# Kernel tuning notes

Measured on AMD Instinct MI355X. Metric: run time of the kernel, lower is better.

## Reference

```python
import jax, jax.numpy as jnp
import numpy as np

RF = 512      # receptive field (power of 2)
F = 128       # filter_size
UP = 200      # upsample_size
MGC = 60      # mgc_size
NB = 4        # num_blocks
NL = 9        # log2(RF) CondConv layers per WaveNet block
T = 4         # number of mgc frames
N = T * UP    # number of sliding windows (800)
SQ = 0.70710678118


def setup_inputs() -> dict:
    key = jax.random.key(0)
    ks = jax.random.split(key, 12)
    r = lambda k, shp, s: jax.random.normal(k, shp, jnp.float32) * s
    return {
        "mgc": r(ks[0], (T, MGC), 1.0),
        "signal": r(ks[1], (N + RF,), 0.5),
        "cond_w": r(ks[2], (MGC * UP, MGC), 0.1),
        "cond_b": jnp.zeros((MGC * UP,), jnp.float32),
        "conv0_w": r(ks[3], (NB, 3, F, 1, 2), 0.3),
        "conv0_b": jnp.zeros((NB, 3, F), jnp.float32),
        "convL_w": r(ks[4], (NB, NL - 1, 3, F, F, 2), 0.08),
        "convL_b": jnp.zeros((NB, NL - 1, 3, F), jnp.float32),
        "condlin_w": r(ks[5], (NB, NL, 2, F, MGC), 0.1),
        "condlin_b": jnp.zeros((NB, NL, 2, F), jnp.float32),
        "pre_w": r(ks[6], (NB, 256, F), 0.08),
        "pre_b": jnp.zeros((NB, 256), jnp.float32),
        "mean_w": r(ks[7], (NB, 1, 256), 0.05),
        "mean_b": jnp.zeros((NB, 1), jnp.float32),
        "std_w": r(ks[8], (NB, 1, 256), 0.05),
        "std_b": jnp.zeros((NB, 1), jnp.float32),
        "eps": r(ks[9], (NB, N, 1), 1.0),
    }


def _cond_conv(h, W, b, cw, cb, cond):
    # h: [N, Cin, L]; W: [3, F, Cin, 2] (input/gate/residual stacked); b: [3, F]
    # kernel=2, stride=2 -> non-overlapping pairs; express as einsum GEMM
    n, c, L = h.shape
    hr = h.reshape(n, c, L // 2, 2)
    o = jnp.einsum('nclk,tock->tnol', hr, W) + b[:, None, :, None]  # [3, N, F, L/2]
    ci = cond @ cw[0].T + cb[0]  # [N, F]
    cg = cond @ cw[1].T + cb[1]  # [N, F]
    it = jnp.tanh(o[0] + ci[:, :, None])
    gt = jax.nn.sigmoid(o[1] + cg[:, :, None])
    return (it * gt + o[2]) * SQ


def _forward(mgc, signal, cond_w, cond_b, conv0_w, conv0_b, convL_w, convL_b,
             condlin_w, condlin_b, pre_w, pre_b, mean_w, mean_b, std_w, std_b, eps):
    # conditioning: Linear(60 -> 60*200) + tanh, reshaped to [T*200, 60]
    cond = jnp.tanh(mgc @ cond_w.T + cond_b).reshape(N, MGC)
    idx = jnp.arange(N)[:, None] + jnp.arange(RF)[None, :]  # sliding windows
    prev = signal
    tails = []
    mean = logvar = None
    for blk in range(NB):
        h = prev[idx][:, None, :]  # [N, 1, RF]
        for l in range(NL):
            W = conv0_w[blk] if l == 0 else convL_w[blk, l - 1]
            bb = conv0_b[blk] if l == 0 else convL_b[blk, l - 1]
            h = _cond_conv(h, W, bb, condlin_w[blk, l], condlin_b[blk, l], cond)
        pre = jax.nn.relu(h[:, :, 0] @ pre_w[blk].T + pre_b[blk])  # [N, 256]
        mean = pre @ mean_w[blk].T + mean_b[blk]    # [N, 1]
        logvar = pre @ std_w[blk].T + std_b[blk]    # [N, 1]
        new_x = eps[blk] * jnp.exp(0.5 * logvar) + mean  # reparameterize
        tails.append(jax.lax.stop_gradient(new_x[-RF:]))  # detached tail
        prev = jnp.concatenate([signal[:RF], new_x[:, 0]])
    return signal[RF:], mean, logvar, jnp.stack(tails)


def reference(mgc, signal, cond_w, cond_b, conv0_w, conv0_b, convL_w, convL_b,
              condlin_w, condlin_b, pre_w, pre_b, mean_w, mean_b, std_w, std_b, eps):
    return _forward(mgc, signal, cond_w, cond_b, conv0_w, conv0_b, convL_w, convL_b,
                    condlin_w, condlin_b, pre_w, pre_b, mean_w, mean_b, std_w, std_b, eps)
```

## Files before the change

kernel.cpp:

```cpp
#include <hip/hip_runtime.h>
#include <hip/hip_bf16.h>

#define F 128
#define MGCS 60
#define NWIN 800
#define RFS 512
#define NBLK 4
#define NLAY 9
#define SQF 0.70710678118f

typedef __attribute__((ext_vector_type(8))) short s16x8;
typedef __attribute__((ext_vector_type(4))) float f32x4;

#define VMCNT(n) asm volatile("s_waitcnt vmcnt(" #n ")" ::: "memory")

__device__ __forceinline__ float gated_act(float o0, float o1, float o2) {
  o0 = fminf(fmaxf(o0, -21.f), 21.f);
  o1 = fminf(fmaxf(o1, -21.f), 21.f);
  float a = __expf(2.f * o0);
  float b = __expf(-o1);
  float r = (a - 1.f) * __builtin_amdgcn_rcpf((a + 1.f) * (1.f + b));
  return (r + o2) * SQF;
}


__global__ void k_cond(const float* __restrict__ mgc, const float* __restrict__ cond_w,
                       const float* __restrict__ cond_b, float* __restrict__ cond) {
  int i = blockIdx.x * blockDim.x + threadIdx.x;
  if (i >= NWIN * MGCS) return;
  int n = i / MGCS, m = i % MGCS;
  int t = n / 200, u = n % 200;
  const float* wrow = cond_w + (size_t)(u * MGCS + m) * MGCS;
  const float* mr = mgc + t * MGCS;
  float s = cond_b[u * MGCS + m];
#pragma unroll
  for (int k = 0; k < MGCS; ++k) s += mr[k] * wrow[k];
  cond[i] = tanhf(s);
}

__global__ __launch_bounds__(256) void k_ci(
    const float* __restrict__ cond, const float* __restrict__ clw,
    const float* __restrict__ clb, float* __restrict__ CI) {
  int w = blockIdx.x;
  int n0 = blockIdx.y * 128;
  __shared__ float wsh[128][61];
  __shared__ float csh[128][61];
  int tid = threadIdx.x;
  for (int idx = tid; idx < 128 * MGCS; idx += 256) {
    int f = idx / MGCS, k = idx % MGCS;
    wsh[f][k] = clw[((size_t)w * 128 + f) * MGCS + k];
  }
  for (int idx = tid; idx < 128 * MGCS; idx += 256) {
    int n = idx / MGCS, k = idx % MGCS;
    csh[n][k] = (n0 + n < NWIN) ? cond[(n0 + n) * MGCS + k] : 0.f;
  }
  __syncthreads();
  int tn = tid >> 4, tf = tid & 15;
  float acc[8][8] = {};
  for (int k = 0; k < MGCS; ++k) {
    float a[8], b[8];
#pragma unroll
    for (int i = 0; i < 8; ++i) a[i] = csh[i * 16 + tn][k];
#pragma unroll
    for (int j = 0; j < 8; ++j) b[j] = wsh[j * 16 + tf][k];
#pragma unroll
    for (int i = 0; i < 8; ++i)
#pragma unroll
      for (int j = 0; j < 8; ++j) acc[i][j] += a[i] * b[j];
  }
  float bb[8];
#pragma unroll
  for (int j = 0; j < 8; ++j) bb[j] = clb[w * 128 + j * 16 + tf];
#pragma unroll
  for (int i = 0; i < 8; ++i) {
    int n = n0 + i * 16 + tn;
    if (n < NWIN) {
#pragma unroll
      for (int j = 0; j < 8; ++j)
        CI[((size_t)w * NWIN + n) * 128 + j * 16 + tf] = acc[i][j] + bb[j];
    }
  }
}

__global__ void k_wt(const float* __restrict__ convL_w, __hip_bfloat16* __restrict__ W2) {
  int i = blockIdx.x * blockDim.x + threadIdx.x;
  const int total = NBLK * 8 * 384 * 256;
  if (i >= total) return;
  int k = i & 255;
  int tf = (i >> 8) % 384;
  int wl = i / (384 * 256);
  int t = tf >> 7, f = tf & 127;
  int k2 = k >> 7, c = k & 127;
  W2[i] = __float2bfloat16(convL_w[(((size_t)(wl * 3 + t) * 128 + f) * 128 + c) * 2 + k2]);
}

__global__ void k_wt2(const float* __restrict__ pre_w, __hip_bfloat16* __restrict__ PW) {
  int i = blockIdx.x * blockDim.x + threadIdx.x;
  if (i < NBLK * 256 * 128) PW[i] = __float2bfloat16(pre_w[i]);
}

__global__ void k_outsig(const float* __restrict__ signal, float* __restrict__ out) {
  int i = blockIdx.x * blockDim.x + threadIdx.x;
  if (i < NWIN) out[i] = signal[RFS + i];
}


__global__ void k_pre0(const float* __restrict__ prev, const float* __restrict__ w0,
                       const float* __restrict__ b0, float* __restrict__ CV) {
  int i = blockIdx.x * blockDim.x + threadIdx.x;
  if (i >= 1310 * 384) return;
  int tf = i % 384, s = i / 384;
  CV[i] = b0[tf] + prev[s] * w0[tf * 2] + prev[s + 1] * w0[tf * 2 + 1];
}

__global__ void k_layer0(const float* __restrict__ CV, const float* __restrict__ CIb,
                         __hip_bfloat16* __restrict__ out) {
  int i = blockIdx.x * blockDim.x + threadIdx.x;
  if (i >= NWIN * 256 * 16) return;
  int fg = i & 15;
  int rest = i >> 4;
  int j = rest & 255;
  int n = rest >> 8;
  int f0 = fg * 8;
  const float* cv = CV + (size_t)(n + 2 * j) * 384;
  const float* ci = CIb + (size_t)n * F;
  float4 c0a = *(const float4*)(cv + f0),       c0b = *(const float4*)(cv + f0 + 4);
  float4 c1a = *(const float4*)(cv + 128 + f0), c1b = *(const float4*)(cv + 132 + f0);
  float4 c2a = *(const float4*)(cv + 256 + f0), c2b = *(const float4*)(cv + 260 + f0);
  float4 i0a = *(const float4*)(ci + f0),       i0b = *(const float4*)(ci + f0 + 4);
  float4 i1a = *(const float4*)(ci + (size_t)NWIN * F + f0);
  float4 i1b = *(const float4*)(ci + (size_t)NWIN * F + f0 + 4);
  s16x8 res;
#pragma unroll
  for (int e = 0; e < 8; ++e) {
    float o0 = ((e < 4) ? (&c0a.x)[e] : (&c0b.x)[e - 4]) + ((e < 4) ? (&i0a.x)[e] : (&i0b.x)[e - 4]);
    float o1 = ((e < 4) ? (&c1a.x)[e] : (&c1b.x)[e - 4]) + ((e < 4) ? (&i1a.x)[e] : (&i1b.x)[e - 4]);
    float o2 = (e < 4) ? (&c2a.x)[e] : (&c2b.x)[e - 4];
    __hip_bfloat16 h = __float2bfloat16(gated_act(o0, o1, o2));
    res[e] = *(short*)&h;
  }
  *(s16x8*)(out + ((size_t)(n * 256 + j)) * F + f0) = res;
}

template <int MFR, int FF, bool FLAT>
__device__ __forceinline__ void fuse_layer(
    const char* src, char* dst, const char* Wb, const float* __restrict__ bb,
    const float* __restrict__ ciA, const float* __restrict__ ciB,
    int n0, int logLW, int MV, int mbase, int fbase, int lane) {
  const int col = lane & 15, kg = lane >> 4;
  f32x4 acc[MFR][FF][3];
#pragma unroll
  for (int mf = 0; mf < MFR; ++mf)
#pragma unroll
    for (int ff = 0; ff < FF; ++ff)
#pragma unroll
      for (int g = 0; g < 3; ++g) acc[mf][ff][g] = (f32x4)(0.f);
#pragma unroll
  for (int ks = 0; ks < 8; ++ks) {
    s16x8 breg[FF][3];
#pragma unroll
    for (int ff = 0; ff < FF; ++ff)
#pragma unroll
      for (int g = 0; g < 3; ++g) {
        int tf = g * 128 + fbase + ff * 16 + col;
        breg[ff][g] = *(const s16x8*)(Wb + (size_t)tf * 512 + ks * 64 + kg * 16);
      }
    s16x8 afr[MFR];
#pragma unroll
    for (int mf = 0; mf < MFR; ++mf) {
      int row = mbase + mf * 16 + col;
      row = row < MV ? row : MV - 1;
      afr[mf] = *(const s16x8*)(src + row * 512 + ((ks * 64 + kg * 16) ^ ((row & 7) << 4)));
    }
#pragma unroll
    for (int ff = 0; ff < FF; ++ff)
#pragma unroll
      for (int g = 0; g < 3; ++g)
#pragma unroll
        for (int mf = 0; mf < MFR; ++mf)
          acc[mf][ff][g] = __builtin_amdgcn_mfma_f32_16x16x32_bf16(afr[mf], breg[ff][g], acc[mf][ff][g], 0, 0, 0);
  }
#pragma unroll
  for (int mf = 0; mf < MFR; ++mf)
#pragma unroll
    for (int ff = 0; ff < FF; ++ff) {
      int f = fbase + ff * 16 + col;
      float b0 = bb[f], b1 = bb[128 + f], b2 = bb[256 + f];
#pragma unroll
      for (int r = 0; r < 4; ++r) {
        int orow = mbase + mf * 16 + kg * 4 + r;
        if (orow < MV) {
          int n = n0 + (orow >> logLW);
          float o0 = acc[mf][ff][0][r] + b0 + ciA[n * 128 + f];
          float o1 = acc[mf][ff][1][r] + b1 + ciB[n * 128 + f];
          float o2 = acc[mf][ff][2][r] + b2;
          __hip_bfloat16 h = __float2bfloat16(gated_act(o0, o1, o2));
          if (FLAT) {
            *(short*)(dst + orow * 256 + ((f * 2) ^ ((orow & 7) << 4))) = *(short*)&h;
          } else {
            int trow = ((orow >> logLW) << (logLW - 1)) | ((orow & ((1 << logLW) - 1)) >> 1);
            int kb = ((orow & 1) * 128 + f) * 2;
            *(short*)(dst + trow * 512 + (kb ^ ((trow & 7) << 4))) = *(short*)&h;
          }
        }
      }
    }
}

__global__ __launch_bounds__(512, 1) void k_fuse12(
    const __hip_bfloat16* __restrict__ A0, const __hip_bfloat16* __restrict__ W2b,
    const float* __restrict__ cb, const float* __restrict__ CIb,
    __hip_bfloat16* __restrict__ outC) {
  __shared__ char Ain[128 * 512];
  __shared__ char Bp[64 * 512];
  const int n = blockIdx.x;
  const int tid = threadIdx.x;
  const int lane = tid & 63, wid = tid >> 6;
  const char* srcg = (const char*)A0 + (size_t)n * 65536;
  const int half = lane >> 5, lin = (lane & 31) * 16;
#pragma unroll
  for (int it = 0; it < 8; ++it) {
    int inst = wid * 8 + it;
    int row = inst * 2 + half;
    __builtin_amdgcn_global_load_lds(
        (const __attribute__((address_space(1))) unsigned int*)(srcg + row * 512 + (lin ^ ((row & 7) << 4))),
        (__attribute__((address_space(3))) unsigned int*)(Ain + inst * 1024), 16, 0, 0);
  }
  VMCNT(0);
  __syncthreads();
  const int fbase = wid * 16;
  const char* W0 = (const char*)W2b;
  const char* W1 = (const char*)W2b + (size_t)384 * 512;
  const float* c1A = CIb + (size_t)(1 * 2 + 0) * NWIN * F;
  const float* c1B = CIb + (size_t)(1 * 2 + 1) * NWIN * F;
  const float* c2A = CIb + (size_t)(2 * 2 + 0) * NWIN * F;
  const float* c2B = CIb + (size_t)(2 * 2 + 1) * NWIN * F;
  fuse_layer<4, 1, false>(Ain, Bp, W0, cb, c1A, c1B, n, 7, 128, 0, fbase, lane);
  fuse_layer<4, 1, false>(Ain, Bp, W0, cb, c1A, c1B, n, 7, 128, 64, fbase, lane);
  __syncthreads();
  fuse_layer<4, 1, true>(Bp, Ain, W1, cb + 384, c2A, c2B, n, 6, 64, 0, fbase, lane);
  __syncthreads();
#pragma unroll
  for (int p = 0; p < 2; ++p) {
    int idx = p * 512 + tid;
    int row = idx >> 4;
    int off = (idx & 15) * 16;
    s16x8 v = *(const s16x8*)(Ain + row * 256 + (off ^ ((row & 7) << 4)));
    *(s16x8*)((char*)outC + (size_t)n * 16384 + row * 256 + off) = v;
  }
}

__global__ __launch_bounds__(256, 1) void k_tail6(
    const __hip_bfloat16* __restrict__ C2, const __hip_bfloat16* __restrict__ W2b,
    const float* __restrict__ cb, const float* __restrict__ CIb,
    const __hip_bfloat16* __restrict__ PWb, const float* __restrict__ pb_,
    const float* __restrict__ mw_, const float* __restrict__ mb_,
    const float* __restrict__ sw_, const float* __restrict__ sb_,
    const float* __restrict__ eps_, const float* __restrict__ signal,
    float* __restrict__ prev_next, float* __restrict__ out_mean,
    float* __restrict__ out_logvar, float* __restrict__ out_tails) {
  __shared__ char Ain[128 * 512];
  __shared__ char Bp[64 * 512];
  __shared__ float psm[4][256];
  __shared__ float psv[4][256];
  const int b = blockIdx.x, n0 = b * 4;
  const int tid = threadIdx.x;
  const int lane = tid & 63, wid = tid >> 6;
  const int col = lane & 15, kg = lane >> 4;
  const char* srcg = (const char*)C2 + (size_t)n0 * 16384;
  const int half = lane >> 5, lin = (lane & 31) * 16;
#pragma unroll
  for (int it = 0; it < 16; ++it) {
    int inst = wid * 16 + it;
    int row = inst * 2 + half;
    __builtin_amdgcn_global_load_lds(
        (const __attribute__((address_space(1))) unsigned int*)(srcg + row * 512 + (lin ^ ((row & 7) << 4))),
        (__attribute__((address_space(3))) unsigned int*)(Ain + inst * 1024), 16, 0, 0);
  }
  VMCNT(0);
  __syncthreads();
  const int fbase = wid * 32;
#define WLp(lm) ((const char*)W2b + (size_t)(lm) * 384 * 512)
#define CIL(l, t) (CIb + (size_t)((l) * 2 + (t)) * NWIN * F)
  fuse_layer<4, 2, false>(Ain, Bp, WLp(2), cb + 2 * 384, CIL(3, 0), CIL(3, 1), n0, 5, 128, 0, fbase, lane);
  fuse_layer<4, 2, false>(Ain, Bp, WLp(2), cb + 2 * 384, CIL(3, 0), CIL(3, 1), n0, 5, 128, 64, fbase, lane);
  __syncthreads();
  fuse_layer<4, 2, false>(Bp, Ain, WLp(3), cb + 3 * 384, CIL(4, 0), CIL(4, 1), n0, 4, 64, 0, fbase, lane);
  __syncthreads();
  fuse_layer<2, 2, false>(Ain, Bp, WLp(4), cb + 4 * 384, CIL(5, 0), CIL(5, 1), n0, 3, 32, 0, fbase, lane);
  __syncthreads();
  fuse_layer<1, 2, false>(Bp, Ain, WLp(5), cb + 5 * 384, CIL(6, 0), CIL(6, 1), n0, 2, 16, 0, fbase, lane);
  __syncthreads();
  fuse_layer<1, 2, false>(Ain, Bp, WLp(6), cb + 6 * 384, CIL(7, 0), CIL(7, 1), n0, 1, 8, 0, fbase, lane);
  __syncthreads();
  fuse_layer<1, 2, true>(Bp, Ain, WLp(7), cb + 7 * 384, CIL(8, 0), CIL(8, 1), n0, 0, 4, 0, fbase, lane);
  __syncthreads();

  {
    f32x4 acc2[4];
#pragma unroll
    for (int nf = 0; nf < 4; ++nf) acc2[nf] = (f32x4)(0.f);
    const char* PB = (const char*)PWb;
    int row = col < 4 ? col : 3;
#pragma unroll
    for (int ks = 0; ks < 4; ++ks) {
      s16x8 afr = *(const s16x8*)(Ain + row * 256 + ((ks * 64 + kg * 16) ^ ((row & 7) << 4)));
#pragma unroll
      for (int nf = 0; nf < 4; ++nf) {
        int o = wid * 64 + nf * 16 + col;
        s16x8 bfr = *(const s16x8*)(PB + (size_t)o * 256 + ks * 64 + kg * 16);
        acc2[nf] = __builtin_amdgcn_mfma_f32_16x16x32_bf16(afr, bfr, acc2[nf], 0, 0, 0);
      }
    }
#pragma unroll
    for (int nf = 0; nf < 4; ++nf) {
      int o = wid * 64 + nf * 16 + col;
      float pb = pb_[o], mw = mw_[o], sw = sw_[o];
#pragma unroll
      for (int r = 0; r < 4; ++r) {
        int m = kg * 4 + r;
        if (m < 4) {
          float p = fmaxf(acc2[nf][r] + pb, 0.f);
          psm[m][o] = p * mw;
          psv[m][o] = p * sw;
        }
      }
    }
  }
  __syncthreads();
  {
    float sm = 0.f, sv = 0.f;
#pragma unroll
    for (int e = 0; e < 4; ++e) {
      sm += psm[wid][lane * 4 + e];
      sv += psv[wid][lane * 4 + e];
    }
#pragma unroll
    for (int off = 32; off > 0; off >>= 1) {
      sm += __shfl_down(sm, off);
      sv += __shfl_down(sv, off);
    }
    if (lane == 0) {
      int nn = n0 + wid;
      float mean = sm + mb_[0];
      float logv = sv + sb_[0];
      float nx = eps_[nn] * expf(0.5f * logv) + mean;
      if (prev_next) prev_next[RFS + nn] = nx;
      if (out_mean) { out_mean[nn] = mean; out_logvar[nn] = logv; }
      if (nn >= NWIN - RFS) out_tails[nn - (NWIN - RFS)] = nx;
    }
  }
  if (prev_next && tid < 4 && n0 + tid < RFS)
    prev_next[n0 + tid] = signal[n0 + tid];
}


extern "C" void kernel_launch(void* const* d_in, const int* in_sizes, int n_in,
                              void* d_out, int out_size, void* d_ws, size_t ws_size,
                              hipStream_t stream) {
  const float* mgc      = (const float*)d_in[0];
  const float* signal   = (const float*)d_in[1];
  const float* cond_w   = (const float*)d_in[2];
  const float* cond_b   = (const float*)d_in[3];
  const float* conv0_w  = (const float*)d_in[4];
  const float* conv0_b  = (const float*)d_in[5];
  const float* convL_w  = (const float*)d_in[6];
  const float* convL_b  = (const float*)d_in[7];
  const float* condlin_w= (const float*)d_in[8];
  const float* condlin_b= (const float*)d_in[9];
  const float* pre_w    = (const float*)d_in[10];
  const float* pre_b    = (const float*)d_in[11];
  const float* mean_w   = (const float*)d_in[12];
  const float* mean_b   = (const float*)d_in[13];
  const float* std_w    = (const float*)d_in[14];
  const float* std_b    = (const float*)d_in[15];
  const float* eps      = (const float*)d_in[16];
  float* out = (float*)d_out;

  float* wsf   = (float*)d_ws;
  float* cond  = wsf;
  float* CI    = cond + 48000;
  float* prevb = CI + 7372800;
  float* CV    = prevb + 5248;
  float* base  = CV + 503040;
  __hip_bfloat16* W2   = (__hip_bfloat16*)base;
  __hip_bfloat16* PW   = W2 + 3145728;
  __hip_bfloat16* bufA = PW + 131072;
  __hip_bfloat16* bufC = bufA + 26214400 + 65536;

  k_cond<<<(NWIN * MGCS + 255) / 256, 256, 0, stream>>>(mgc, cond_w, cond_b, cond);
  k_ci<<<dim3(72, 7), 256, 0, stream>>>(cond, condlin_w, condlin_b, CI);
  k_wt<<<(NBLK * 8 * 384 * 256 + 255) / 256, 256, 0, stream>>>(convL_w, W2);
  k_wt2<<<(NBLK * 256 * 128 + 255) / 256, 256, 0, stream>>>(pre_w, PW);
  k_outsig<<<(NWIN + 255) / 256, 256, 0, stream>>>(signal, out);

  for (int blk = 0; blk < NBLK; ++blk) {
    const float* prev = (blk == 0) ? signal : (prevb + (size_t)(blk - 1) * 1312);
    const float* CIb = CI + (size_t)(blk * NLAY) * 2 * NWIN * F;
    k_pre0<<<(1310 * 384 + 255) / 256, 256, 0, stream>>>(
        prev, conv0_w + (size_t)blk * 3 * F * 2, conv0_b + (size_t)blk * 3 * F, CV);
    k_layer0<<<(NWIN * 256 * 16 + 255) / 256, 256, 0, stream>>>(CV, CIb, bufA);

    k_fuse12<<<NWIN, 512, 0, stream>>>(
        bufA, W2 + (size_t)blk * 8 * 384 * 256, convL_b + (size_t)blk * 8 * 384, CIb, bufC);

    k_tail6<<<NWIN / 4, 256, 0, stream>>>(
        bufC, W2 + (size_t)blk * 8 * 384 * 256,
        convL_b + (size_t)blk * 8 * 384, CIb,
        PW + (size_t)blk * 256 * 128, pre_b + (size_t)blk * 256,
        mean_w + (size_t)blk * 256, mean_b + blk,
        std_w + (size_t)blk * 256, std_b + blk,
        eps + (size_t)blk * NWIN, signal,
        (blk < 3) ? (prevb + (size_t)blk * 1312) : nullptr,
        (blk == 3) ? (out + 800) : nullptr,
        (blk == 3) ? (out + 1600) : nullptr,
        out + 2400 + (size_t)blk * 512);
  }
}
```

Before: 677.9 us.

## Fuse layer0 gated activation into fused kernel and halve per-block work

Removes the standalone layer0 kernel and computes its gated activation directly into shared memory inside a new k_fuse012 kernel. This avoids writing and re-reading a large bf16 intermediate buffer in global memory. Each window is now split across two blocks with half-size LDS tiles so more blocks fit per CU. The tail kernel likewise processes two windows per block instead of four, giving more blocks and higher occupancy bounds. The cost is duplicated weight loads across the extra blocks and more launch-level parallelism overhead.

```diff
diff --git a/kernel.cpp b/kernel.cpp
--- a/kernel.cpp
+++ b/kernel.cpp
@@ -111,35 +111,6 @@
   if (i >= 1310 * 384) return;
   int tf = i % 384, s = i / 384;
   CV[i] = b0[tf] + prev[s] * w0[tf * 2] + prev[s + 1] * w0[tf * 2 + 1];
-}
-
-__global__ void k_layer0(const float* __restrict__ CV, const float* __restrict__ CIb,
-                         __hip_bfloat16* __restrict__ out) {
-  int i = blockIdx.x * blockDim.x + threadIdx.x;
-  if (i >= NWIN * 256 * 16) return;
-  int fg = i & 15;
-  int rest = i >> 4;
-  int j = rest & 255;
-  int n = rest >> 8;
-  int f0 = fg * 8;
-  const float* cv = CV + (size_t)(n + 2 * j) * 384;
-  const float* ci = CIb + (size_t)n * F;
-  float4 c0a = *(const float4*)(cv + f0),       c0b = *(const float4*)(cv + f0 + 4);
-  float4 c1a = *(const float4*)(cv + 128 + f0), c1b = *(const float4*)(cv + 132 + f0);
-  float4 c2a = *(const float4*)(cv + 256 + f0), c2b = *(const float4*)(cv + 260 + f0);
-  float4 i0a = *(const float4*)(ci + f0),       i0b = *(const float4*)(ci + f0 + 4);
-  float4 i1a = *(const float4*)(ci + (size_t)NWIN * F + f0);
-  float4 i1b = *(const float4*)(ci + (size_t)NWIN * F + f0 + 4);
-  s16x8 res;
-#pragma unroll
-  for (int e = 0; e < 8; ++e) {
-    float o0 = ((e < 4) ? (&c0a.x)[e] : (&c0b.x)[e - 4]) + ((e < 4) ? (&i0a.x)[e] : (&i0b.x)[e - 4]);
-    float o1 = ((e < 4) ? (&c1a.x)[e] : (&c1b.x)[e - 4]) + ((e < 4) ? (&i1a.x)[e] : (&i1b.x)[e - 4]);
-    float o2 = (e < 4) ? (&c2a.x)[e] : (&c2b.x)[e - 4];
-    __hip_bfloat16 h = __float2bfloat16(gated_act(o0, o1, o2));
-    res[e] = *(short*)&h;
-  }
-  *(s16x8*)(out + ((size_t)(n * 256 + j)) * F + f0) = res;
 }
 
 template <int MFR, int FF, bool FLAT>
@@ -207,50 +178,64 @@
     }
 }
 
-__global__ __launch_bounds__(512, 1) void k_fuse12(
-    const __hip_bfloat16* __restrict__ A0, const __hip_bfloat16* __restrict__ W2b,
+#define CIL(l, t) (CIb + (size_t)((l) * 2 + (t)) * NWIN * F)
+
+__global__ __launch_bounds__(512, 4) void k_fuse012(
+    const float* __restrict__ CV, const __hip_bfloat16* __restrict__ W2b,
     const float* __restrict__ cb, const float* __restrict__ CIb,
     __hip_bfloat16* __restrict__ outC) {
-  __shared__ char Ain[128 * 512];
-  __shared__ char Bp[64 * 512];
-  const int n = blockIdx.x;
+  __shared__ char Ain[64 * 512];
+  __shared__ char Bp[32 * 512];
+  const int bx = blockIdx.x;
+  const int n = bx >> 1, c = bx & 1;
   const int tid = threadIdx.x;
   const int lane = tid & 63, wid = tid >> 6;
-  const char* srcg = (const char*)A0 + (size_t)n * 65536;
-  const int half = lane >> 5, lin = (lane & 31) * 16;
-#pragma unroll
-  for (int it = 0; it < 8; ++it) {
-    int inst = wid * 8 + it;
-    int row = inst * 2 + half;
-    __builtin_amdgcn_global_load_lds(
-        (const __attribute__((address_space(1))) unsigned int*)(srcg + row * 512 + (lin ^ ((row & 7) << 4))),
-        (__attribute__((address_space(3))) unsigned int*)(Ain + inst * 1024), 16, 0, 0);
-  }
-  VMCNT(0);
-  __syncthreads();
+
+  {
+    const int jl = tid >> 2;
+    const int f0 = (tid & 3) * 32;
+    const float* cv = CV + (size_t)(n + 2 * (c * 128 + jl)) * 384;
+    const float* ci0 = CIL(0, 0) + n * 128;
+    const float* ci1 = CIL(0, 1) + n * 128;
+    const int row = jl >> 1;
+    const int kbase = (jl & 1) * 128;
+#pragma unroll
+    for (int e8 = 0; e8 < 4; ++e8) {
+      int f = f0 + e8 * 8;
+      float4 a0 = *(const float4*)(cv + f),       a1 = *(const float4*)(cv + f + 4);
+      float4 b0 = *(const float4*)(cv + 128 + f), b1 = *(const float4*)(cv + 132 + f);
+      float4 g0 = *(const float4*)(cv + 256 + f), g1 = *(const float4*)(cv + 260 + f);
+      float4 i0 = *(const float4*)(ci0 + f),      i0b = *(const float4*)(ci0 + f + 4);
+      float4 i1 = *(const float4*)(ci1 + f),      i1b = *(const float4*)(ci1 + f + 4);
+      s16x8 res;
+#pragma unroll
+      for (int e = 0; e < 8; ++e) {
+        float o0 = ((e < 4) ? (&a0.x)[e] : (&a1.x)[e - 4]) + ((e < 4) ? (&i0.x)[e] : (&i0b.x)[e - 4]);
+        float o1 = ((e < 4) ? (&b0.x)[e] : (&b1.x)[e - 4]) + ((e < 4) ? (&i1.x)[e] : (&i1b.x)[e - 4]);
+        float o2 = (e < 4) ? (&g0.x)[e] : (&g1.x)[e - 4];
+        __hip_bfloat16 h = __float2bfloat16(gated_act(o0, o1, o2));
+        res[e] = *(short*)&h;
+      }
+      *(s16x8*)(Ain + row * 512 + (((kbase + f) * 2) ^ ((row & 7) << 4))) = res;
+    }
+  }
+  __syncthreads();
+
   const int fbase = wid * 16;
-  const char* W0 = (const char*)W2b;
-  const char* W1 = (const char*)W2b + (size_t)384 * 512;
-  const float* c1A = CIb + (size_t)(1 * 2 + 0) * NWIN * F;
-  const float* c1B = CIb + (size_t)(1 * 2 + 1) * NWIN * F;
-  const float* c2A = CIb + (size_t)(2 * 2 + 0) * NWIN * F;
-  const float* c2B = CIb + (size_t)(2 * 2 + 1) * NWIN * F;
-  fuse_layer<4, 1, false>(Ain, Bp, W0, cb, c1A, c1B, n, 7, 128, 0, fbase, lane);
-  fuse_layer<4, 1, false>(Ain, Bp, W0, cb, c1A, c1B, n, 7, 128, 64, fbase, lane);
-  __syncthreads();
-  fuse_layer<4, 1, true>(Bp, Ain, W1, cb + 384, c2A, c2B, n, 6, 64, 0, fbase, lane);
-  __syncthreads();
-#pragma unroll
-  for (int p = 0; p < 2; ++p) {
-    int idx = p * 512 + tid;
-    int row = idx >> 4;
-    int off = (idx & 15) * 16;
-    s16x8 v = *(const s16x8*)(Ain + row * 256 + (off ^ ((row & 7) << 4)));
-    *(s16x8*)((char*)outC + (size_t)n * 16384 + row * 256 + off) = v;
-  }
-}
-
-__global__ __launch_bounds__(256, 1) void k_tail6(
+  fuse_layer<4, 1, false>(Ain, Bp, (const char*)W2b, cb,
+                          CIL(1, 0), CIL(1, 1), n, 30, 64, 0, fbase, lane);
+  __syncthreads();
+  fuse_layer<2, 1, true>(Bp, Ain, (const char*)W2b + (size_t)384 * 512, cb + 384,
+                         CIL(2, 0), CIL(2, 1), n, 30, 32, 0, fbase, lane);
+  __syncthreads();
+  {
+    int r2 = tid >> 4, off = (tid & 15) * 16;
+    s16x8 v = *(const s16x8*)(Ain + r2 * 256 + (off ^ ((r2 & 7) << 4)));
+    *(s16x8*)((char*)outC + (size_t)n * 16384 + (c * 32 + r2) * 256 + off) = v;
+  }
+}
+
+__global__ __launch_bounds__(256, 3) void k_tail6(
     const __hip_bfloat16* __restrict__ C2, const __hip_bfloat16* __restrict__ W2b,
     const float* __restrict__ cb, const float* __restrict__ CIb,
     const __hip_bfloat16* __restrict__ PWb, const float* __restrict__ pb_,
@@ -259,19 +244,19 @@
     const float* __restrict__ eps_, const float* __restrict__ signal,
     float* __restrict__ prev_next, float* __restrict__ out_mean,
     float* __restrict__ out_logvar, float* __restrict__ out_tails) {
-  __shared__ char Ain[128 * 512];
-  __shared__ char Bp[64 * 512];
-  __shared__ float psm[4][256];
-  __shared__ float psv[4][256];
-  const int b = blockIdx.x, n0 = b * 4;
+  __shared__ char Ain[64 * 512];
+  __shared__ char Bp[32 * 512];
+  __shared__ float psm[2][256];
+  __shared__ float psv[2][256];
+  const int b = blockIdx.x, n0 = b * 2;
   const int tid = threadIdx.x;
   const int lane = tid & 63, wid = tid >> 6;
   const int col = lane & 15, kg = lane >> 4;
   const char* srcg = (const char*)C2 + (size_t)n0 * 16384;
   const int half = lane >> 5, lin = (lane & 31) * 16;
 #pragma unroll
-  for (int it = 0; it < 16; ++it) {
-    int inst = wid * 16 + it;
+  for (int it = 0; it < 8; ++it) {
+    int inst = wid * 8 + it;
     int row = inst * 2 + half;
     __builtin_amdgcn_global_load_lds(
         (const __attribute__((address_space(1))) unsigned int*)(srcg + row * 512 + (lin ^ ((row & 7) << 4))),
@@ -281,19 +266,17 @@
   __syncthreads();
   const int fbase = wid * 32;
 #define WLp(lm) ((const char*)W2b + (size_t)(lm) * 384 * 512)
-#define CIL(l, t) (CIb + (size_t)((l) * 2 + (t)) * NWIN * F)
-  fuse_layer<4, 2, false>(Ain, Bp, WLp(2), cb + 2 * 384, CIL(3, 0), CIL(3, 1), n0, 5, 128, 0, fbase, lane);
-  fuse_layer<4, 2, false>(Ain, Bp, WLp(2), cb + 2 * 384, CIL(3, 0), CIL(3, 1), n0, 5, 128, 64, fbase, lane);
-  __syncthreads();
-  fuse_layer<4, 2, false>(Bp, Ain, WLp(3), cb + 3 * 384, CIL(4, 0), CIL(4, 1), n0, 4, 64, 0, fbase, lane);
-  __syncthreads();
-  fuse_layer<2, 2, false>(Ain, Bp, WLp(4), cb + 4 * 384, CIL(5, 0), CIL(5, 1), n0, 3, 32, 0, fbase, lane);
-  __syncthreads();
-  fuse_layer<1, 2, false>(Bp, Ain, WLp(5), cb + 5 * 384, CIL(6, 0), CIL(6, 1), n0, 2, 16, 0, fbase, lane);
-  __syncthreads();
-  fuse_layer<1, 2, false>(Ain, Bp, WLp(6), cb + 6 * 384, CIL(7, 0), CIL(7, 1), n0, 1, 8, 0, fbase, lane);
-  __syncthreads();
-  fuse_layer<1, 2, true>(Bp, Ain, WLp(7), cb + 7 * 384, CIL(8, 0), CIL(8, 1), n0, 0, 4, 0, fbase, lane);
+  fuse_layer<4, 2, false>(Ain, Bp, WLp(2), cb + 2 * 384, CIL(3, 0), CIL(3, 1), n0, 5, 64, 0, fbase, lane);
+  __syncthreads();
+  fuse_layer<2, 2, false>(Bp, Ain, WLp(3), cb + 3 * 384, CIL(4, 0), CIL(4, 1), n0, 4, 32, 0, fbase, lane);
+  __syncthreads();
+  fuse_layer<1, 2, false>(Ain, Bp, WLp(4), cb + 4 * 384, CIL(5, 0), CIL(5, 1), n0, 3, 16, 0, fbase, lane);
+  __syncthreads();
+  fuse_layer<1, 2, false>(Bp, Ain, WLp(5), cb + 5 * 384, CIL(6, 0), CIL(6, 1), n0, 2, 8, 0, fbase, lane);
+  __syncthreads();
+  fuse_layer<1, 2, false>(Ain, Bp, WLp(6), cb + 6 * 384, CIL(7, 0), CIL(7, 1), n0, 1, 4, 0, fbase, lane);
+  __syncthreads();
+  fuse_layer<1, 2, true>(Bp, Ain, WLp(7), cb + 7 * 384, CIL(8, 0), CIL(8, 1), n0, 0, 2, 0, fbase, lane);
   __syncthreads();
 
   {
@@ -301,7 +284,7 @@
 #pragma unroll
     for (int nf = 0; nf < 4; ++nf) acc2[nf] = (f32x4)(0.f);
     const char* PB = (const char*)PWb;
-    int row = col < 4 ? col : 3;
+    int row = col < 2 ? col : 1;
 #pragma unroll
     for (int ks = 0; ks < 4; ++ks) {
       s16x8 afr = *(const s16x8*)(Ain + row * 256 + ((ks * 64 + kg * 16) ^ ((row & 7) << 4)));
@@ -319,7 +302,7 @@
 #pragma unroll
       for (int r = 0; r < 4; ++r) {
         int m = kg * 4 + r;
-        if (m < 4) {
+        if (m < 2) {
           float p = fmaxf(acc2[nf][r] + pb, 0.f);
           psm[m][o] = p * mw;
           psv[m][o] = p * sw;
@@ -328,7 +311,7 @@
     }
   }
   __syncthreads();
-  {
+  if (wid < 2) {
     float sm = 0.f, sv = 0.f;
 #pragma unroll
     for (int e = 0; e < 4; ++e) {
@@ -350,7 +333,7 @@
       if (nn >= NWIN - RFS) out_tails[nn - (NWIN - RFS)] = nx;
     }
   }
-  if (prev_next && tid < 4 && n0 + tid < RFS)
+  if (prev_next && tid < 2 && n0 + tid < RFS)
     prev_next[n0 + tid] = signal[n0 + tid];
 }
 
@@ -385,8 +368,7 @@
   float* base  = CV + 503040;
   __hip_bfloat16* W2   = (__hip_bfloat16*)base;
   __hip_bfloat16* PW   = W2 + 3145728;
-  __hip_bfloat16* bufA = PW + 131072;
-  __hip_bfloat16* bufC = bufA + 26214400 + 65536;
+  __hip_bfloat16* bufC = PW + 131072;
 
   k_cond<<<(NWIN * MGCS + 255) / 256, 256, 0, stream>>>(mgc, cond_w, cond_b, cond);
   k_ci<<<dim3(72, 7), 256, 0, stream>>>(cond, condlin_w, condlin_b, CI);
@@ -399,12 +381,11 @@
     const float* CIb = CI + (size_t)(blk * NLAY) * 2 * NWIN * F;
     k_pre0<<<(1310 * 384 + 255) / 256, 256, 0, stream>>>(
         prev, conv0_w + (size_t)blk * 3 * F * 2, conv0_b + (size_t)blk * 3 * F, CV);
-    k_layer0<<<(NWIN * 256 * 16 + 255) / 256, 256, 0, stream>>>(CV, CIb, bufA);
-
-    k_fuse12<<<NWIN, 512, 0, stream>>>(
-        bufA, W2 + (size_t)blk * 8 * 384 * 256, convL_b + (size_t)blk * 8 * 384, CIb, bufC);
-
-    k_tail6<<<NWIN / 4, 256, 0, stream>>>(
+
+    k_fuse012<<<NWIN * 2, 512, 0, stream>>>(
+        CV, W2 + (size_t)blk * 8 * 384 * 256, convL_b + (size_t)blk * 8 * 384, CIb, bufC);
+
+    k_tail6<<<NWIN / 2, 256, 0, stream>>>(
         bufC, W2 + (size_t)blk * 8 * 384 * 256,
         convL_b + (size_t)blk * 8 * 384, CIb,
         PW + (size_t)blk * 256 * 128, pre_b + (size_t)blk * 256,
```

Measured after the change: 942.0 us. 1.39x slower.
